# Optimization experiments

Measured on AMD Instinct MI355X. Metric: run time of the kernel, lower is better.

## Reference

```python
import jax, jax.numpy as jnp
import numpy as np

N = 100000   # nodes
E = 400000   # edges
G = 1024     # graphs in batch
IN = 4; H = 128; HD = 4; DH = H // HD; L = 3; ED = 4; FF = 2 * H; JK = H * L
SCALE = 1.0 / np.sqrt(DH).astype(np.float32)


def _ln(x, g, b):
    m = x.mean(-1, keepdims=True)
    v = x.var(-1, keepdims=True)
    return (x - m) / jnp.sqrt(v + 1e-5) * g + b


def setup_inputs() -> dict:
    key = jax.random.key(0)
    ks = jax.random.split(key, 24)
    rn = lambda k, s, sc=0.05: jax.random.normal(k, s, jnp.float32) * sc
    return {
        "x": rn(ks[0], (N, IN), 1.0),
        "edge_index": jax.random.randint(ks[1], (2, E), 0, N),
        "edge_attr": rn(ks[2], (E, ED), 1.0),
        "batch": jnp.sort(jax.random.randint(ks[3], (N,), 0, G)),
        "u": rn(ks[4], (G, 1), 1.0),
        "Win": rn(ks[5], (IN, H)), "b_in": jnp.zeros(H),
        "Wq": rn(ks[6], (L, H, H)), "bq": jnp.zeros((L, H)),
        "Wk": rn(ks[7], (L, H, H)), "bk": jnp.zeros((L, H)),
        "Wv": rn(ks[8], (L, H, H)), "bv": jnp.zeros((L, H)),
        "We": rn(ks[9], (L, ED, H)),
        "Wskip": rn(ks[10], (L, H, H)), "bskip": jnp.zeros((L, H)),
        "ln1_g": jnp.ones((L, H)), "ln1_b": jnp.zeros((L, H)),
        "Wf1": rn(ks[11], (L, H, FF)), "bf1": jnp.zeros((L, FF)),
        "Wf2": rn(ks[12], (L, FF, H)), "bf2": jnp.zeros((L, H)),
        "ln2_g": jnp.ones((L, H)), "ln2_b": jnp.zeros((L, H)),
        "Wg1": rn(ks[13], (JK, H)), "bg1": jnp.zeros(H),
        "Wg2": rn(ks[14], (H, 1)), "bg2": jnp.zeros(1),
        "Wh1": rn(ks[15], (JK + 1, H)), "bh1": jnp.zeros(H),
        "Wh2": rn(ks[16], (H, 3)), "bh2": jnp.zeros(3),
    }


def reference(x, edge_index, edge_attr, batch, u,
              Win, b_in, Wq, bq, Wk, bk, Wv, bv, We, Wskip, bskip,
              ln1_g, ln1_b, Wf1, bf1, Wf2, bf2, ln2_g, ln2_b,
              Wg1, bg1, Wg2, bg2, Wh1, bh1, Wh2, bh2):
    src, dst = edge_index[0], edge_index[1]
    h = x @ Win + b_in                                   # [N,H]
    xs = []
    for l in range(L):
        q = (h @ Wq[l] + bq[l]).reshape(N, HD, DH)
        k_n = h @ Wk[l] + bk[l]
        v_n = h @ Wv[l] + bv[l]
        e = edge_attr @ We[l]                            # [E,H] edge bias
        ke = (k_n[src] + e).reshape(E, HD, DH)
        ve = (v_n[src] + e).reshape(E, HD, DH)
        logits = (q[dst] * ke).sum(-1) * SCALE           # [E,HD]
        m = jax.ops.segment_max(logits, dst, N)
        p = jnp.exp(logits - m[dst])
        s = jax.ops.segment_sum(p, dst, N)
        alpha = p / (s[dst] + 1e-16)                     # segment softmax per dst node
        agg = jax.ops.segment_sum(alpha[:, :, None] * ve, dst, N).reshape(N, H)
        attn = agg + h @ Wskip[l] + bskip[l]             # root weight (skip lin)
        h = _ln(h + attn, ln1_g[l], ln1_b[l])
        ff = jax.nn.relu(h @ Wf1[l] + bf1[l]) @ Wf2[l] + bf2[l]
        h = _ln(h + ff, ln2_g[l], ln2_b[l])
        xs.append(h)
    xc = jnp.concatenate(xs, -1)                         # JumpingKnowledge 'cat' [N,JK]
    gate = (jax.nn.relu(xc @ Wg1 + bg1) @ Wg2 + bg2)[:, 0]  # [N]
    gm = jax.ops.segment_max(gate, batch, G)
    gp = jnp.exp(gate - gm[batch])
    gs = jax.ops.segment_sum(gp, batch, G)
    w = gp / (gs[batch] + 1e-16)                         # per-graph softmax
    pooled = jax.ops.segment_sum(w[:, None] * xc, batch, G)  # [G,JK]
    out = jnp.concatenate([pooled, u], 1)                # [G,JK+1]
    return jax.nn.relu(out @ Wh1 + bh1) @ Wh2 + bh2      # [G,3]
```

## Files before the change

### kernel.cpp

```cpp
#include <hip/hip_runtime.h>
#include <math.h>

#define H 128
#define LAYERS 3
#define FFDIM 256
#define JK 384
#define ATT_SCALE 0.17677669529663687f

typedef unsigned short u16;
typedef __attribute__((ext_vector_type(4))) float f32x4;
typedef __attribute__((ext_vector_type(8))) short short8;
typedef __attribute__((ext_vector_type(8))) unsigned short ushort8v;

static inline int cdiv(int a, int b) { return (a + b - 1) / b; }

static __device__ __forceinline__ float bf2f(u16 u) {
    union { unsigned int i; float f; } v; v.i = ((unsigned int)u) << 16; return v.f;
}
static __device__ __forceinline__ u16 f2bf(float f) {
    union { float f; unsigned int i; } v; v.f = f;
    unsigned int r = v.i + 0x7FFFu + ((v.i >> 16) & 1u);
    return (u16)(r >> 16);
}

__global__ void hist_kernel(const int* __restrict__ ei, int* __restrict__ counts, int E) {
    int e = blockIdx.x * blockDim.x + threadIdx.x;
    if (e >= E) return;
    atomicAdd(&counts[ei[E + e]], 1);
}

__global__ __launch_bounds__(256) void scan1_kernel(const int* __restrict__ counts,
                                                    int* __restrict__ offsets,
                                                    int* __restrict__ bsum, int N) {
    __shared__ int sh[256];
    int t = threadIdx.x;
    int base = blockIdx.x * 1024 + t * 4;
    int v0 = 0, v1 = 0, v2 = 0, v3 = 0;
    if (base + 3 < N) {
        int4 q = *(const int4*)&counts[base];
        v0 = q.x; v1 = q.y; v2 = q.z; v3 = q.w;
    } else {
        if (base < N) v0 = counts[base];
        if (base + 1 < N) v1 = counts[base + 1];
        if (base + 2 < N) v2 = counts[base + 2];
        if (base + 3 < N) v3 = counts[base + 3];
    }
    int ts = v0 + v1 + v2 + v3;
    sh[t] = ts; __syncthreads();
    for (int off = 1; off < 256; off <<= 1) {
        int x = (t >= off) ? sh[t - off] : 0;
        __syncthreads(); sh[t] += x; __syncthreads();
    }
    int excl = sh[t] - ts;
    if (base < N)     offsets[base]     = excl;
    if (base + 1 < N) offsets[base + 1] = excl + v0;
    if (base + 2 < N) offsets[base + 2] = excl + v0 + v1;
    if (base + 3 < N) offsets[base + 3] = excl + v0 + v1 + v2;
    if (t == 255) bsum[blockIdx.x] = sh[255];
}

__global__ __launch_bounds__(128) void scan2_kernel(const int* __restrict__ bsum,
                                                    int* __restrict__ boffs,
                                                    int* __restrict__ offsets, int nb, int N) {
    __shared__ int sh[128];
    int t = threadIdx.x;
    int s = (t < nb) ? bsum[t] : 0;
    sh[t] = s; __syncthreads();
    for (int off = 1; off < 128; off <<= 1) {
        int x = (t >= off) ? sh[t - off] : 0;
        __syncthreads(); sh[t] += x; __syncthreads();
    }
    if (t < nb) boffs[t] = sh[t] - s;
    if (t == 0) offsets[N] = sh[nb - 1];
}

__global__ __launch_bounds__(256) void scan3_kernel(int* __restrict__ offsets,
                                                    const int* __restrict__ boffs, int N) {
    int add = boffs[blockIdx.x];
    int base = blockIdx.x * 1024 + threadIdx.x * 4;
#pragma unroll
    for (int i = 0; i < 4; ++i)
        if (base + i < N) offsets[base + i] += add;
}

__global__ void scatter_kernel(const int* __restrict__ ei, const float* __restrict__ eattr,
                               const int* __restrict__ offsets,
                               int* __restrict__ cursor, int* __restrict__ psrc,
                               float4* __restrict__ pe, int E) {
    int e = blockIdx.x * blockDim.x + threadIdx.x;
    if (e >= E) return;
    int d = ei[E + e];
    int pos = atomicAdd(&cursor[d], 1);
    int o = offsets[d] + pos;
    psrc[o] = ei[e];
    pe[o] = *(const float4*)&eattr[(size_t)e * 4];
}

__global__ void graph_bounds_kernel(const int* __restrict__ batch, int* __restrict__ gstart,
                                    int N, int G) {
    int g = blockIdx.x * blockDim.x + threadIdx.x;
    if (g > G) return;
    int lo = 0, hi = N;
    while (lo < hi) { int mid = (lo + hi) >> 1; if (batch[mid] < g) lo = mid + 1; else hi = mid; }
    gstart[g] = lo;
}

struct TD { const float* src; int dstoff, K, N; };
struct TA { TD d[19]; };

__global__ __launch_bounds__(256) void wconv_kernel(TA a, u16* __restrict__ WT) {
    TD d = a.d[blockIdx.y];
    int i = blockIdx.x * 256 + threadIdx.x;
    int tot = d.K * d.N;
    if (i >= tot) return;
    int c = i / d.K, k = i - c * d.K;
    WT[d.dstoff + i] = f2bf(d.src[(size_t)k * d.N + c]);
}

__global__ __launch_bounds__(256) void input_proj_kernel(const float* __restrict__ x,
                                                         const float* __restrict__ Win,
                                                         const float* __restrict__ b_in,
                                                         u16* __restrict__ h, int ldh, int N) {
    int idx = blockIdx.x * 256 + threadIdx.x;
    int n = idx >> 6, c = (idx & 63) * 2;
    if (n >= N) return;
    float4 xv = *(const float4*)&x[(size_t)n * 4];
    float o0 = b_in[c]     + xv.x * Win[c]     + xv.y * Win[H + c]     + xv.z * Win[2 * H + c]     + xv.w * Win[3 * H + c];
    float o1 = b_in[c + 1] + xv.x * Win[c + 1] + xv.y * Win[H + c + 1] + xv.z * Win[2 * H + c + 1] + xv.w * Win[3 * H + c + 1];
    ushort2 s; s.x = f2bf(o0); s.y = f2bf(o1);
    *(ushort2*)&h[(size_t)n * ldh + c] = s;
}

__device__ __forceinline__ void stage_tile(const u16* __restrict__ g, int ld, int row0,
                                           int nrows, int kt, u16* __restrict__ sm, int t) {
#pragma unroll
    for (int i = 0; i < 4; ++i) {
        int f = i * 256 + t;
        int row = f >> 3, ck = f & 7;
        int n = row0 + row; if (n >= nrows) n = nrows - 1;
        uint4 v = *(const uint4*)(g + (size_t)n * ld + kt + ck * 8);
        int sw = ck ^ (row & 7);
        *(uint4*)(sm + row * 64 + sw * 8) = v;
    }
}

template <int MODE, int NBY>
__global__ __launch_bounds__(256) void gemm_mfma(
    const u16* __restrict__ A, int lda,
    const u16* __restrict__ WT, int K,
    const float* __restrict__ b0, const float* __restrict__ b1,
    const float* __restrict__ b2, const float* __restrict__ b3,
    const float* __restrict__ resid,
    u16* __restrict__ obf, float* __restrict__ of32,
    int nrows)
{
    alignas(16) __shared__ char smemraw[33792];
    u16* Asm = (u16*)smemraw;
    u16* Bsm = (u16*)(smemraw + 16384);
    float* stage = (float*)smemraw;
    int t = threadIdx.x;
    int lane = t & 63, wid = t >> 6;
    int wr = wid >> 1, wc = wid & 1;

    int T = gridDim.x, id = blockIdx.x;
    int qd = T >> 3, rr = T & 7;
    int xcd = id & 7, pos = id >> 3;
    int swz = (xcd < rr ? xcd * (qd + 1) : rr * (qd + 1) + (xcd - rr) * qd) + pos;
    int by = swz & (NBY - 1);
    int row0 = (swz / NBY) * 128;

    const u16* WTb = WT + (size_t)by * 128 * K;

    f32x4 acc[4][4] = {};

    for (int kt = 0; kt < K; kt += 64) {
        stage_tile(A, lda, row0, nrows, kt, Asm, t);
        stage_tile(WTb, K, 0, 128, kt, Bsm, t);
        __syncthreads();
        int g = lane >> 4;
        int l15 = lane & 15;
#pragma unroll
        for (int kk = 0; kk < 2; ++kk) {
            int cb = kk * 4 + g;
            short8 af[4], bf[4];
#pragma unroll
            for (int mi = 0; mi < 4; ++mi) {
                int r = wr * 64 + mi * 16 + l15;
                af[mi] = *(const short8*)(Asm + r * 64 + ((cb ^ (r & 7)) * 8));
            }
#pragma unroll
            for (int nj = 0; nj < 4; ++nj) {
                int c = wc * 64 + nj * 16 + l15;
                bf[nj] = *(const short8*)(Bsm + c * 64 + ((cb ^ (c & 7)) * 8));
            }
#pragma unroll
            for (int mi = 0; mi < 4; ++mi)
#pragma unroll
                for (int nj = 0; nj < 4; ++nj)
                    acc[mi][nj] = __builtin_amdgcn_mfma_f32_16x16x32_bf16(af[mi], bf[nj], acc[mi][nj], 0, 0, 0);
        }
        __syncthreads();
    }

    int g = lane >> 4, l15 = lane & 15;

    if (MODE == 3) {
        float* gsum = (float*)Asm;
        float part[4][4];
#pragma unroll
        for (int mi = 0; mi < 4; ++mi)
#pragma unroll
            for (int r = 0; r < 4; ++r) part[mi][r] = 0.f;
#pragma unroll
        for (int nj = 0; nj < 4; ++nj) {
            int col = wc * 64 + nj * 16 + l15;
            float bb = b0[col];
            float w2 = b1[col];
#pragma unroll
            for (int mi = 0; mi < 4; ++mi)
#pragma unroll
                for (int r = 0; r < 4; ++r) {
                    float v = fmaxf(acc[mi][nj][r] + bb, 0.f);
                    part[mi][r] = fmaf(v, w2, part[mi][r]);
                }
        }
#pragma unroll
        for (int off = 1; off <= 8; off <<= 1)
#pragma unroll
            for (int mi = 0; mi < 4; ++mi)
#pragma unroll
                for (int r = 0; r < 4; ++r) part[mi][r] += __shfl_xor(part[mi][r], off);
        if (wc == 0 && l15 == 0) {
#pragma unroll
            for (int mi = 0; mi < 4; ++mi)
#pragma unroll
                for (int r = 0; r < 4; ++r)
                    gsum[wr * 64 + mi * 16 + g * 4 + r] = part[mi][r];
        }
        __syncthreads();
        if (wc == 1 && l15 == 0) {
            float bg2v = b2[0];
#pragma unroll
            for (int mi = 0; mi < 4; ++mi)
#pragma unroll
                for (int r = 0; r < 4; ++r) {
                    int lr = wr * 64 + mi * 16 + g * 4 + r;
                    int n = row0 + lr;
                    if (n < nrows) of32[n] = part[mi][r] + gsum[lr] + bg2v;
                }
        }
        return;
    }

    const float* bias;
    u16* ob = nullptr; float* of = nullptr;
    if (MODE == 0) {
        bias = (by == 0) ? b0 : (by == 1) ? b1 : (by == 2) ? b2 : b3;
        if (by < 3) ob = obf + by * 128; else of = of32;
    } else if (MODE == 1) {
        bias = b0 + by * 128;
        ob = obf + by * 128;
    } else {
        bias = b0;
        of = of32;
    }

#pragma unroll
    for (int p = 0; p < 2; ++p) {
        if (wr == p) {
#pragma unroll
            for (int nj = 0; nj < 4; ++nj) {
                int col = wc * 64 + nj * 16 + l15;
                float bb = bias[col];
#pragma unroll
                for (int mi = 0; mi < 4; ++mi)
#pragma unroll
                    for (int r = 0; r < 4; ++r) {
                        float v = acc[mi][nj][r] + bb;
                        if (MODE == 1) v = fmaxf(v, 0.f);
                        stage[(mi * 16 + g * 4 + r) * 132 + col] = v;
                    }
            }
        }
        __syncthreads();
        if (ob) {
#pragma unroll
            for (int it = 0; it < 4; ++it) {
                int lr = it * 16 + (t >> 4);
                int gr = row0 + p * 64 + lr;
                if (gr < nrows) {
                    int c8 = l15 * 8;
                    ushort8v o;
#pragma unroll
                    for (int i = 0; i < 8; ++i) o[i] = f2bf(stage[lr * 132 + c8 + i]);
                    *(ushort8v*)&ob[(size_t)gr * 384 + c8] = o;
                }
            }
        } else {
            int l31 = t & 31;
#pragma unroll
            for (int it = 0; it < 8; ++it) {
                int lr = it * 8 + (t >> 5);
                int gr = row0 + p * 64 + lr;
                if (gr < nrows) {
                    int c4 = l31 * 4;
                    float4 v = *(float4*)&stage[lr * 132 + c4];
                    if (MODE == 2) {
                        float4 rv = *(const float4*)&resid[(size_t)gr * 128 + c4];
                        v.x += rv.x; v.y += rv.y; v.z += rv.z; v.w += rv.w;
                    }
                    *(float4*)&of[(size_t)gr * 128 + c4] = v;
                }
            }
        }
        __syncthreads();
    }
}

__global__ __launch_bounds__(256) void attn_kernel(
    u16* __restrict__ qkv,
    const u16* __restrict__ h_in, int ld_h,
    const int* __restrict__ offsets,
    const int* __restrict__ psrc, const float4* __restrict__ pe,
    const float* __restrict__ We_l,
    const float* __restrict__ g1, const float* __restrict__ b1,
    float* __restrict__ hmid, int N)
{
    int tid = threadIdx.x;
    int grp = tid >> 4;
    int sub = tid & 15;
    int n = blockIdx.x * 16 + grp;
    if (n >= N) return;
    int d0 = sub * 8;

    float we[4][8];
#pragma unroll
    for (int aa = 0; aa < 4; ++aa) {
        float4 w0 = *(const float4*)&We_l[aa * H + d0];
        float4 w1 = *(const float4*)&We_l[aa * H + d0 + 4];
        we[aa][0] = w0.x; we[aa][1] = w0.y; we[aa][2] = w0.z; we[aa][3] = w0.w;
        we[aa][4] = w1.x; we[aa][5] = w1.y; we[aa][6] = w1.z; we[aa][7] = w1.w;
    }

    ushort8v qraw = *(const ushort8v*)&qkv[(size_t)n * JK + d0];
    float qf[8];
#pragma unroll
    for (int i = 0; i < 8; ++i) qf[i] = bf2f(qraw[i]);

    float m = -INFINITY, ssum = 0.f;
    float a[8] = {0.f, 0.f, 0.f, 0.f, 0.f, 0.f, 0.f, 0.f};
    int e0 = offsets[n], e1 = offsets[n + 1];
    for (int j = e0; j < e1; ++j) {
        int s = psrc[j];
        float4 ea = pe[j];
        const u16* srow = qkv + (size_t)s * JK;
        ushort8v kraw = *(const ushort8v*)&srow[H + d0];
        ushort8v vraw = *(const ushort8v*)&srow[2 * H + d0];
        float part = 0.f, vv[8];
#pragma unroll
        for (int i = 0; i < 8; ++i) {
            float eb = ea.x * we[0][i] + ea.y * we[1][i] + ea.z * we[2][i] + ea.w * we[3][i];
            float kf = bf2f(kraw[i]) + eb;
            vv[i] = bf2f(vraw[i]) + eb;
            part = fmaf(qf[i], kf, part);
        }
        part += __shfl_xor(part, 1);
        part += __shfl_xor(part, 2);
        float logit = part * ATT_SCALE;
        float mn = fmaxf(m, logit);
        float corr = __expf(m - mn);
        float p = __expf(logit - mn);
        ssum = ssum * corr + p;
#pragma unroll
        for (int i = 0; i < 8; ++i) a[i] = a[i] * corr + p * vv[i];
        m = mn;
    }
    float inv = 1.f / (ssum + 1e-16f);

    ushort8v hraw = *(const ushort8v*)&h_in[(size_t)n * ld_h + d0];
    float4 sk0 = *(const float4*)&hmid[(size_t)n * H + d0];
    float4 sk1 = *(const float4*)&hmid[(size_t)n * H + d0 + 4];
    float skf[8] = {sk0.x, sk0.y, sk0.z, sk0.w, sk1.x, sk1.y, sk1.z, sk1.w};
    float tv[8], sum = 0.f, sq = 0.f;
#pragma unroll
    for (int i = 0; i < 8; ++i) {
        tv[i] = bf2f(hraw[i]) + a[i] * inv + skf[i];
        sum += tv[i]; sq += tv[i] * tv[i];
    }
#pragma unroll
    for (int off = 1; off <= 8; off <<= 1) { sum += __shfl_xor(sum, off); sq += __shfl_xor(sq, off); }
    float mean = sum * (1.f / 128.f);
    float var = sq * (1.f / 128.f) - mean * mean;
    float rstd = rsqrtf(var + 1e-5f);
    float4 ga = *(const float4*)&g1[d0];
    float4 gb = *(const float4*)&g1[d0 + 4];
    float4 ba = *(const float4*)&b1[d0];
    float4 bb = *(const float4*)&b1[d0 + 4];
    float gg[8] = {ga.x, ga.y, ga.z, ga.w, gb.x, gb.y, gb.z, gb.w};
    float bbv[8] = {ba.x, ba.y, ba.z, ba.w, bb.x, bb.y, bb.z, bb.w};
    float o[8];
    ushort8v obv;
#pragma unroll
    for (int i = 0; i < 8; ++i) {
        o[i] = (tv[i] - mean) * rstd * gg[i] + bbv[i];
        obv[i] = f2bf(o[i]);
    }
    *(float4*)&hmid[(size_t)n * H + d0]     = make_float4(o[0], o[1], o[2], o[3]);
    *(float4*)&hmid[(size_t)n * H + d0 + 4] = make_float4(o[4], o[5], o[6], o[7]);
    *(ushort8v*)&qkv[(size_t)n * JK + d0] = obv;
}

__global__ __launch_bounds__(256) void ln_kernel(const float* __restrict__ in,
                                                 const float* __restrict__ g,
                                                 const float* __restrict__ b,
                                                 u16* __restrict__ out, int ldo, int N) {
    int wid = threadIdx.x >> 6;
    int lane = threadIdx.x & 63;
    int n = blockIdx.x * 4 + wid;
    if (n >= N) return;
    int d0 = lane * 2;
    float2 t = *(const float2*)&in[(size_t)n * H + d0];
    float sum = t.x + t.y, sq = t.x * t.x + t.y * t.y;
#pragma unroll
    for (int off = 32; off; off >>= 1) { sum += __shfl_xor(sum, off); sq += __shfl_xor(sq, off); }
    float mean = sum * (1.f / 128.f);
    float var = sq * (1.f / 128.f) - mean * mean;
    float rstd = rsqrtf(var + 1e-5f);
    ushort2 s;
    s.x = f2bf((t.x - mean) * rstd * g[d0] + b[d0]);
    s.y = f2bf((t.y - mean) * rstd * g[d0 + 1] + b[d0 + 1]);
    *(ushort2*)&out[(size_t)n * ldo + d0] = s;
}

#define PCH 512
__global__ __launch_bounds__(256) void pool_kernel(const float* __restrict__ gate,
                                                   const u16* __restrict__ xc,
                                                   const int* __restrict__ gstart,
                                                   const float* __restrict__ u,
                                                   float* __restrict__ pooled, int G) {
    int g = blockIdx.x;
    int t = threadIdx.x;
    int s0 = gstart[g], s1 = gstart[g + 1];
    __shared__ float red[256];
    __shared__ float w[PCH];
    float mx = -INFINITY;
    for (int i = s0 + t; i < s1; i += 256) mx = fmaxf(mx, gate[i]);
    red[t] = mx; __syncthreads();
    for (int off = 128; off; off >>= 1) { if (t < off) red[t] = fmaxf(red[t], red[t + off]); __syncthreads(); }
    float gm = red[0]; __syncthreads();
    float sm = 0.f;
    for (int i = s0 + t; i < s1; i += 256) sm += __expf(gate[i] - gm);
    red[t] = sm; __syncthreads();
    for (int off = 128; off; off >>= 1) { if (t < off) red[t] += red[t + off]; __syncthreads(); }
    float inv = 1.f / (red[0] + 1e-16f);
    float acc0 = 0.f, acc1 = 0.f;
    for (int base = s0; base < s1; base += PCH) {
        int cnt = min(PCH, s1 - base);
        __syncthreads();
        for (int i = t; i < cnt; i += 256) w[i] = __expf(gate[base + i] - gm) * inv;
        __syncthreads();
        for (int c = 0; c < cnt; ++c) {
            const u16* row = xc + (size_t)(base + c) * JK;
            float wc = w[c];
            acc0 = fmaf(wc, bf2f(row[t]), acc0);
            if (t < 128) acc1 = fmaf(wc, bf2f(row[t + 256]), acc1);
        }
    }
    pooled[(size_t)g * (JK + 1) + t] = acc0;
    if (t < 128) pooled[(size_t)g * (JK + 1) + t + 256] = acc1;
    if (t == 0) pooled[(size_t)g * (JK + 1) + JK] = u[g];
}

__global__ __launch_bounds__(128) void head_kernel(const float* __restrict__ pooled,
                                                   const float* __restrict__ Wh1,
                                                   const float* __restrict__ bh1,
                                                   const float* __restrict__ Wh2,
                                                   const float* __restrict__ bh2,
                                                   float* __restrict__ out, int G) {
    int g = blockIdx.x;
    int j = threadIdx.x;
    __shared__ float hid[128];
    float acc = bh1[j];
    const float* pr = pooled + (size_t)g * (JK + 1);
    for (int k = 0; k < JK + 1; ++k) acc = fmaf(pr[k], Wh1[(size_t)k * H + j], acc);
    hid[j] = fmaxf(acc, 0.f);
    __syncthreads();
    if (j < 3) {
        float o = bh2[j];
        for (int k = 0; k < H; ++k) o += hid[k] * Wh2[k * 3 + j];
        out[(size_t)g * 3 + j] = o;
    }
}

extern "C" void kernel_launch(void* const* d_in, const int* in_sizes, int n_in,
                              void* d_out, int out_size, void* d_ws, size_t ws_size,
                              hipStream_t stream) {
    const float* x     = (const float*)d_in[0];
    const int*   ei    = (const int*)d_in[1];
    const float* eattr = (const float*)d_in[2];
    const int*   batch = (const int*)d_in[3];
    const float* u     = (const float*)d_in[4];
    const float* Win   = (const float*)d_in[5];
    const float* b_in  = (const float*)d_in[6];
    const float* Wq    = (const float*)d_in[7];
    const float* bq    = (const float*)d_in[8];
    const float* Wk    = (const float*)d_in[9];
    const float* bk    = (const float*)d_in[10];
    const float* Wv    = (const float*)d_in[11];
    const float* bv    = (const float*)d_in[12];
    const float* We    = (const float*)d_in[13];
    const float* Wskip = (const float*)d_in[14];
    const float* bskip = (const float*)d_in[15];
    const float* ln1_g = (const float*)d_in[16];
    const float* ln1_b = (const float*)d_in[17];
    const float* Wf1   = (const float*)d_in[18];
    const float* bf1   = (const float*)d_in[19];
    const float* Wf2   = (const float*)d_in[20];
    const float* bf2   = (const float*)d_in[21];
    const float* ln2_g = (const float*)d_in[22];
    const float* ln2_b = (const float*)d_in[23];
    const float* Wg1   = (const float*)d_in[24];
    const float* bg1   = (const float*)d_in[25];
    const float* Wg2   = (const float*)d_in[26];
    const float* bg2   = (const float*)d_in[27];
    const float* Wh1   = (const float*)d_in[28];
    const float* bh1   = (const float*)d_in[29];
    const float* Wh2   = (const float*)d_in[30];
    const float* bh2   = (const float*)d_in[31];

    const int N = in_sizes[3];
    const int E = in_sizes[1] / 2;
    const int G = in_sizes[4];

    char* p = (char*)d_ws;
    auto alloc = [&](size_t bytes) { char* r = p; p += (bytes + 255) & ~(size_t)255; return r; };
    int*    counts  = (int*)alloc((size_t)N * 4);
    int*    cursor  = (int*)alloc((size_t)N * 4);
    int*    offsets = (int*)alloc((size_t)(N + 1) * 4);
    int*    psrc    = (int*)alloc((size_t)E * 4);
    float4* pe      = (float4*)alloc((size_t)E * 16);
    int*    gstart  = (int*)alloc((size_t)(G + 1) * 4);
    int*    bsum    = (int*)alloc(128 * 4);
    int*    boffs   = (int*)alloc(128 * 4);
    float*  gate    = (float*)alloc((size_t)N * 4);
    float*  pooled  = (float*)alloc((size_t)G * (JK + 1) * 4);
    u16*    WT      = (u16*)alloc((size_t)442368 * 2);
    float*  hmid    = (float*)alloc((size_t)N * H * 4);
    u16*    xc      = (u16*)alloc((size_t)N * JK * 2);
    u16*    qkv     = (u16*)alloc((size_t)N * JK * 2);

    const int QKVS_OFF = 0;
    const int F1_OFF   = 3 * 65536;
    const int F2_OFF   = F1_OFF + 3 * 32768;
    const int G1_OFF   = F2_OFF + 3 * 32768;

    hipMemsetAsync(counts, 0, (size_t)N * 4, stream);
    hipMemsetAsync(cursor, 0, (size_t)N * 4, stream);

    int eb = cdiv(E, 256);
    int nb = cdiv(N, 1024);
    hist_kernel<<<eb, 256, 0, stream>>>(ei, counts, E);
    scan1_kernel<<<nb, 256, 0, stream>>>(counts, offsets, bsum, N);
    scan2_kernel<<<1, 128, 0, stream>>>(bsum, boffs, offsets, nb, N);
    scan3_kernel<<<nb, 256, 0, stream>>>(offsets, boffs, N);
    scatter_kernel<<<eb, 256, 0, stream>>>(ei, eattr, offsets, cursor, psrc, pe, E);
    graph_bounds_kernel<<<cdiv(G + 1, 256), 256, 0, stream>>>(batch, gstart, N, G);

    TA ta;
    for (int l = 0; l < 3; ++l) {
        ta.d[l * 4 + 0] = { Wq    + (size_t)l * 16384, QKVS_OFF + l * 65536 + 0,     128, 128 };
        ta.d[l * 4 + 1] = { Wk    + (size_t)l * 16384, QKVS_OFF + l * 65536 + 16384, 128, 128 };
        ta.d[l * 4 + 2] = { Wv    + (size_t)l * 16384, QKVS_OFF + l * 65536 + 32768, 128, 128 };
        ta.d[l * 4 + 3] = { Wskip + (size_t)l * 16384, QKVS_OFF + l * 65536 + 49152, 128, 128 };
        ta.d[12 + l]    = { Wf1   + (size_t)l * 32768, F1_OFF   + l * 32768,         128, 256 };
        ta.d[15 + l]    = { Wf2   + (size_t)l * 32768, F2_OFF   + l * 32768,         256, 128 };
    }
    ta.d[18] = { Wg1, G1_OFF, 384, 128 };
    dim3 wg(cdiv(49152, 256), 19);
    wconv_kernel<<<wg, 256, 0, stream>>>(ta, WT);

    input_proj_kernel<<<cdiv(N * 64, 256), 256, 0, stream>>>(x, Win, b_in, xc, JK, N);

    int gb = cdiv(N, 128);
    int nb16 = cdiv(N, 16);
    int nb4 = cdiv(N, 4);
    for (int l = 0; l < LAYERS; ++l) {
        const u16* hin = xc + (size_t)((l == 0) ? 0 : (l - 1) * H);
        gemm_mfma<0, 4><<<gb * 4, 256, 0, stream>>>(
            hin, JK, WT + QKVS_OFF + (size_t)l * 65536, 128,
            bq + l * H, bk + l * H, bv + l * H, bskip + l * H,
            nullptr, qkv, hmid, N);
        attn_kernel<<<nb16, 256, 0, stream>>>(qkv, hin, JK, offsets, psrc, pe,
                                              We + (size_t)l * 4 * H, ln1_g + l * H, ln1_b + l * H,
                                              hmid, N);
        gemm_mfma<1, 2><<<gb * 2, 256, 0, stream>>>(
            qkv, JK, WT + F1_OFF + (size_t)l * 32768, 128,
            bf1 + (size_t)l * FFDIM, nullptr, nullptr, nullptr,
            nullptr, qkv + H, nullptr, N);
        gemm_mfma<2, 1><<<gb, 256, 0, stream>>>(
            qkv + H, JK, WT + F2_OFF + (size_t)l * 32768, 256,
            bf2 + (size_t)l * H, nullptr, nullptr, nullptr,
            hmid, nullptr, hmid, N);
        ln_kernel<<<nb4, 256, 0, stream>>>(hmid, ln2_g + l * H, ln2_b + l * H,
                                           xc + (size_t)l * H, JK, N);
    }

    gemm_mfma<3, 1><<<gb, 256, 0, stream>>>(
        xc, JK, WT + G1_OFF, JK,
        bg1, Wg2, bg2, nullptr,
        nullptr, nullptr, gate, N);
    pool_kernel<<<G, 256, 0, stream>>>(gate, xc, gstart, u, pooled, G);
    head_kernel<<<G, 128, 0, stream>>>(pooled, Wh1, bh1, Wh2, bh2, (float*)d_out, G);
}
```

Measured before the change: 724.8 us.

## Factor edge bias out of attention loop and store skip/residual in bf16

The edge-feature bias is refactored algebraically. q·We is precomputed once per node, so each logit only needs a 4-term dot with edge_attr. The value-side bias is accumulated as a softmax-weighted edge_attr sum and projected once after the loop. The skip projection output and the attention residual are now kept in bf16 instead of fp32: the skip goes to a bf16 buffer and the FF2 residual is read from the bf16 LN1 output in qkv. Together these cut per-edge ALU work and fp32 memory traffic, at the cost of slightly lower precision in the skip and residual paths.

```diff
diff --git a/kernel.cpp b/kernel.cpp
--- a/kernel.cpp
+++ b/kernel.cpp
@@ -150,8 +150,8 @@
     const u16* __restrict__ WT, int K,
     const float* __restrict__ b0, const float* __restrict__ b1,
     const float* __restrict__ b2, const float* __restrict__ b3,
-    const float* __restrict__ resid,
-    u16* __restrict__ obf, float* __restrict__ of32,
+    const u16* __restrict__ resid16,
+    u16* __restrict__ obf, u16* __restrict__ obf2, float* __restrict__ of32,
     int nrows)
 {
     alignas(16) __shared__ char smemraw[33792];
@@ -253,10 +253,11 @@
     }
 
     const float* bias;
-    u16* ob = nullptr; float* of = nullptr;
+    u16* ob = nullptr; int ldob = 384; float* of = nullptr;
     if (MODE == 0) {
         bias = (by == 0) ? b0 : (by == 1) ? b1 : (by == 2) ? b2 : b3;
-        if (by < 3) ob = obf + by * 128; else of = of32;
+        if (by < 3) ob = obf + by * 128;
+        else { ob = obf2; ldob = 128; }
     } else if (MODE == 1) {
         bias = b0 + by * 128;
         ob = obf + by * 128;
@@ -293,7 +294,7 @@
                     ushort8v o;
 #pragma unroll
                     for (int i = 0; i < 8; ++i) o[i] = f2bf(stage[lr * 132 + c8 + i]);
-                    *(ushort8v*)&ob[(size_t)gr * 384 + c8] = o;
+                    *(ushort8v*)&ob[(size_t)gr * ldob + c8] = o;
                 }
             }
         } else {
@@ -306,8 +307,8 @@
                     int c4 = l31 * 4;
                     float4 v = *(float4*)&stage[lr * 132 + c4];
                     if (MODE == 2) {
-                        float4 rv = *(const float4*)&resid[(size_t)gr * 128 + c4];
-                        v.x += rv.x; v.y += rv.y; v.z += rv.z; v.w += rv.w;
+                        ushort4 rv = *(const ushort4*)&resid16[(size_t)gr * 384 + c4];
+                        v.x += bf2f(rv.x); v.y += bf2f(rv.y); v.z += bf2f(rv.z); v.w += bf2f(rv.w);
                     }
                     *(float4*)&of[(size_t)gr * 128 + c4] = v;
                 }
@@ -320,11 +321,12 @@
 __global__ __launch_bounds__(256) void attn_kernel(
     u16* __restrict__ qkv,
     const u16* __restrict__ h_in, int ld_h,
+    const u16* __restrict__ skipb,
     const int* __restrict__ offsets,
     const int* __restrict__ psrc, const float4* __restrict__ pe,
     const float* __restrict__ We_l,
     const float* __restrict__ g1, const float* __restrict__ b1,
-    float* __restrict__ hmid, int N)
+    int N)
 {
     int tid = threadIdx.x;
     int grp = tid >> 4;
@@ -347,8 +349,20 @@
 #pragma unroll
     for (int i = 0; i < 8; ++i) qf[i] = bf2f(qraw[i]);
 
+    float qe[4];
+#pragma unroll
+    for (int aa = 0; aa < 4; ++aa) {
+        float s = 0.f;
+#pragma unroll
+        for (int i = 0; i < 8; ++i) s = fmaf(qf[i], we[aa][i], s);
+        s += __shfl_xor(s, 1);
+        s += __shfl_xor(s, 2);
+        qe[aa] = s;
+    }
+
     float m = -INFINITY, ssum = 0.f;
     float a[8] = {0.f, 0.f, 0.f, 0.f, 0.f, 0.f, 0.f, 0.f};
+    float ws0 = 0.f, ws1 = 0.f, ws2 = 0.f, ws3 = 0.f;
     int e0 = offsets[n], e1 = offsets[n + 1];
     for (int j = e0; j < e1; ++j) {
         int s = psrc[j];
@@ -356,35 +370,35 @@
         const u16* srow = qkv + (size_t)s * JK;
         ushort8v kraw = *(const ushort8v*)&srow[H + d0];
         ushort8v vraw = *(const ushort8v*)&srow[2 * H + d0];
-        float part = 0.f, vv[8];
-#pragma unroll
-        for (int i = 0; i < 8; ++i) {
-            float eb = ea.x * we[0][i] + ea.y * we[1][i] + ea.z * we[2][i] + ea.w * we[3][i];
-            float kf = bf2f(kraw[i]) + eb;
-            vv[i] = bf2f(vraw[i]) + eb;
-            part = fmaf(qf[i], kf, part);
-        }
+        float part = 0.f;
+#pragma unroll
+        for (int i = 0; i < 8; ++i) part = fmaf(qf[i], bf2f(kraw[i]), part);
         part += __shfl_xor(part, 1);
         part += __shfl_xor(part, 2);
-        float logit = part * ATT_SCALE;
+        float logit = (part + ea.x * qe[0] + ea.y * qe[1] + ea.z * qe[2] + ea.w * qe[3]) * ATT_SCALE;
         float mn = fmaxf(m, logit);
         float corr = __expf(m - mn);
         float p = __expf(logit - mn);
         ssum = ssum * corr + p;
 #pragma unroll
-        for (int i = 0; i < 8; ++i) a[i] = a[i] * corr + p * vv[i];
+        for (int i = 0; i < 8; ++i) a[i] = a[i] * corr + p * bf2f(vraw[i]);
+        ws0 = ws0 * corr + p * ea.x;
+        ws1 = ws1 * corr + p * ea.y;
+        ws2 = ws2 * corr + p * ea.z;
+        ws3 = ws3 * corr + p * ea.w;
         m = mn;
     }
     float inv = 1.f / (ssum + 1e-16f);
+#pragma unroll
+    for (int i = 0; i < 8; ++i)
+        a[i] += ws0 * we[0][i] + ws1 * we[1][i] + ws2 * we[2][i] + ws3 * we[3][i];
 
     ushort8v hraw = *(const ushort8v*)&h_in[(size_t)n * ld_h + d0];
-    float4 sk0 = *(const float4*)&hmid[(size_t)n * H + d0];
-    float4 sk1 = *(const float4*)&hmid[(size_t)n * H + d0 + 4];
-    float skf[8] = {sk0.x, sk0.y, sk0.z, sk0.w, sk1.x, sk1.y, sk1.z, sk1.w};
+    ushort8v skraw = *(const ushort8v*)&skipb[(size_t)n * H + d0];
     float tv[8], sum = 0.f, sq = 0.f;
 #pragma unroll
     for (int i = 0; i < 8; ++i) {
-        tv[i] = bf2f(hraw[i]) + a[i] * inv + skf[i];
+        tv[i] = bf2f(hraw[i]) + a[i] * inv + bf2f(skraw[i]);
         sum += tv[i]; sq += tv[i] * tv[i];
     }
 #pragma unroll
@@ -398,15 +412,10 @@
     float4 bb = *(const float4*)&b1[d0 + 4];
     float gg[8] = {ga.x, ga.y, ga.z, ga.w, gb.x, gb.y, gb.z, gb.w};
     float bbv[8] = {ba.x, ba.y, ba.z, ba.w, bb.x, bb.y, bb.z, bb.w};
-    float o[8];
     ushort8v obv;
 #pragma unroll
-    for (int i = 0; i < 8; ++i) {
-        o[i] = (tv[i] - mean) * rstd * gg[i] + bbv[i];
-        obv[i] = f2bf(o[i]);
-    }
-    *(float4*)&hmid[(size_t)n * H + d0]     = make_float4(o[0], o[1], o[2], o[3]);
-    *(float4*)&hmid[(size_t)n * H + d0 + 4] = make_float4(o[4], o[5], o[6], o[7]);
+    for (int i = 0; i < 8; ++i)
+        obv[i] = f2bf((tv[i] - mean) * rstd * gg[i] + bbv[i]);
     *(ushort8v*)&qkv[(size_t)n * JK + d0] = obv;
 }
 
@@ -546,6 +555,7 @@
     float*  pooled  = (float*)alloc((size_t)G * (JK + 1) * 4);
     u16*    WT      = (u16*)alloc((size_t)442368 * 2);
     float*  hmid    = (float*)alloc((size_t)N * H * 4);
+    u16*    skipb   = (u16*)hmid;
     u16*    xc      = (u16*)alloc((size_t)N * JK * 2);
     u16*    qkv     = (u16*)alloc((size_t)N * JK * 2);
 
@@ -589,18 +599,18 @@
         gemm_mfma<0, 4><<<gb * 4, 256, 0, stream>>>(
             hin, JK, WT + QKVS_OFF + (size_t)l * 65536, 128,
             bq + l * H, bk + l * H, bv + l * H, bskip + l * H,
-            nullptr, qkv, hmid, N);
-        attn_kernel<<<nb16, 256, 0, stream>>>(qkv, hin, JK, offsets, psrc, pe,
+            nullptr, qkv, skipb, nullptr, N);
+        attn_kernel<<<nb16, 256, 0, stream>>>(qkv, hin, JK, skipb, offsets, psrc, pe,
                                               We + (size_t)l * 4 * H, ln1_g + l * H, ln1_b + l * H,
-                                              hmid, N);
+                                              N);
         gemm_mfma<1, 2><<<gb * 2, 256, 0, stream>>>(
             qkv, JK, WT + F1_OFF + (size_t)l * 32768, 128,
             bf1 + (size_t)l * FFDIM, nullptr, nullptr, nullptr,
-            nullptr, qkv + H, nullptr, N);
+            nullptr, qkv + H, nullptr, nullptr, N);
         gemm_mfma<2, 1><<<gb, 256, 0, stream>>>(
             qkv + H, JK, WT + F2_OFF + (size_t)l * 32768, 256,
             bf2 + (size_t)l * H, nullptr, nullptr, nullptr,
-            hmid, nullptr, hmid, N);
+            qkv, nullptr, nullptr, hmid, N);
         ln_kernel<<<nb4, 256, 0, stream>>>(hmid, ln2_g + l * H, ln2_b + l * H,
                                            xc + (size_t)l * H, JK, N);
     }
@@ -608,7 +618,7 @@
     gemm_mfma<3, 1><<<gb, 256, 0, stream>>>(
         xc, JK, WT + G1_OFF, JK,
         bg1, Wg2, bg2, nullptr,
-        nullptr, nullptr, gate, N);
+        nullptr, nullptr, nullptr, gate, N);
     pool_kernel<<<G, 256, 0, stream>>>(gate, xc, gstart, u, pooled, G);
     head_kernel<<<G, 128, 0, stream>>>(pooled, Wh1, bh1, Wh2, bh2, (float*)d_out, G);
 }
```

After: 702.1 us. 1.03x faster.
